# Performance work log

Measured on AMD Instinct MI355X. Metric: run time of the kernel, lower is better.

The kernel has to match this reference:

```python
import jax, jax.numpy as jnp
import numpy as np

B, T, D_IN, D_OUT = 4, 2048, 1024, 1024


def setup_inputs() -> dict:
    key = jax.random.key(0)
    k1, k2, k3, k4 = jax.random.split(key, 4)
    s_in = 1.0 / np.sqrt(D_IN)
    return {
        "input_vector": jax.random.normal(k1, (B, T, D_IN), dtype=jnp.float32),
        "w_q": jax.random.normal(k2, (D_IN, D_OUT), dtype=jnp.float32) * s_in,
        "w_k": jax.random.normal(k3, (D_IN, D_OUT), dtype=jnp.float32) * s_in,
        "w_v": jax.random.normal(k4, (D_IN, D_OUT), dtype=jnp.float32) * s_in,
    }


def reference(input_vector, w_q, w_k, w_v):
    # projections: [B, T, D_OUT]
    q = jnp.einsum("btd,de->bte", input_vector, w_q)
    k = jnp.einsum("btd,de->bte", input_vector, w_k)
    v = jnp.einsum("btd,de->bte", input_vector, w_v)

    T_ = q.shape[1]
    # raw scores [B, T, T]
    scores = jnp.einsum("bqd,bkd->bqk", q, k)
    # causal mask (strict upper triangle masked to -inf), applied BEFORE scaling
    # (as in the original; -inf is invariant under the scale anyway)
    causal = jnp.tril(jnp.ones((T_, T_), dtype=bool))  # True = keep
    scores = jnp.where(causal[None, :, :], scores, -jnp.inf)
    scores = scores / jnp.sqrt(jnp.asarray(k.shape[-1], scores.dtype))
    attn = jax.nn.softmax(scores, axis=-1)
    # dropout = 0.0 (eval): identity
    return jnp.einsum("bqk,bkd->bqd", attn, v)
```

## Files before the change

kernel.cpp:

```cpp
#include <hip/hip_runtime.h>
#include <cstdint>
#include <math.h>

typedef unsigned short u16;
typedef __attribute__((ext_vector_type(8))) short short8;
typedef __attribute__((ext_vector_type(16))) float f32x16;

__device__ __forceinline__ u16 f2bf(float f) {
  uint32_t u = __float_as_uint(f);
  u += 0x7FFFu + ((u >> 16) & 1u);
  return (u16)(u >> 16);
}
__device__ __forceinline__ float bf2f(u16 h) {
  return __uint_as_float(((uint32_t)h) << 16);
}

__device__ __forceinline__ void async_ld16(u16* lds, const u16* g) {
  __builtin_amdgcn_global_load_lds((const __attribute__((address_space(1))) uint32_t*)g,
                                   (__attribute__((address_space(3))) uint32_t*)lds,
                                   16, 0, 0);
}

template <bool OUT_BF16, int MODE, bool KLIM>
__global__ __launch_bounds__(256) void gemm_bt(
    const u16* __restrict__ A, int lda, long zsA,
    const u16* __restrict__ B, int ldb, long zsB,
    void* __restrict__ Cv, int ldc, long zsC,
    int K, float scale, int NB)
{
  const int b = blockIdx.x, zb = blockIdx.y;
  int nb, mb;
  if constexpr (MODE == 1) {
    const int u = b & 7, v = b >> 3;
    nb = v & (NB - 1);
    mb = u * ((int)(gridDim.x >> 3) / NB) + (v / NB);
  } else if constexpr (MODE == 2) {
    const int u = b & 7, idx = b >> 3;
    if (idx <= u) { mb = u;      nb = idx; }
    else          { mb = 15 - u; nb = idx - u - 1; }
  } else if constexpr (MODE == 3) {
    const int u = b & 7, idx = b >> 3;
    mb = (idx < 8) ? u : 15 - u;
    nb = idx & 7;
  } else {
    nb = b % NB;
    mb = b / NB;
  }

  A += (long)zb * zsA;
  B += (long)zb * zsB;
  const int m0 = mb * 128, n0 = nb * 128;

  __shared__ __align__(16) u16 lsA[128 * 32];
  __shared__ __align__(16) u16 lsB[128 * 32];

  const int tid = threadIdx.x;
  const int lane = tid & 63;
  const int wave = tid >> 6;
  const int wr = (wave >> 1) * 64;
  const int wc = (wave & 1) * 64;

  f32x16 acc[2][2];
#pragma unroll
  for (int i = 0; i < 2; ++i)
#pragma unroll
    for (int j = 0; j < 2; ++j)
#pragma unroll
      for (int r = 0; r < 16; ++r) acc[i][j][r] = 0.f;

  const int c0 = tid;
  const int c1 = tid + 256;
  const int r0 = c0 >> 2, q0 = (((c0 & 3) ^ (r0 & 3))) * 8;
  const int r1 = c1 >> 2, q1 = (((c1 & 3) ^ (r1 & 3))) * 8;

  const int klim = (mb + 1) * 128;
  const int kmax = KLIM ? (K < klim ? K : klim) : K;

  const u16* pA0 = A + (long)(m0 + r0) * lda + q0;
  const u16* pA1 = A + (long)(m0 + r1) * lda + q1;
  const u16* pB0 = B + (long)(n0 + r0) * ldb + q0;
  const u16* pB1 = B + (long)(n0 + r1) * ldb + q1;

  const int m32 = lane & 31;
  const int hh = lane >> 5;
  const int sw = lane & 3;
  int offA[2][2], offB[2][2];
#pragma unroll
  for (int i = 0; i < 2; ++i)
#pragma unroll
    for (int ks = 0; ks < 2; ++ks) {
      const int kq = ((ks << 1) | hh) ^ sw;
      offA[i][ks] = (wr + i * 32 + m32) * 32 + kq * 8;
      offB[i][ks] = (wc + i * 32 + m32) * 32 + kq * 8;
    }

  for (int k0 = 0; k0 < kmax; k0 += 32) {
    __syncthreads();
    async_ld16(&lsA[c0 * 8], pA0);
    async_ld16(&lsA[c1 * 8], pA1);
    async_ld16(&lsB[c0 * 8], pB0);
    async_ld16(&lsB[c1 * 8], pB1);
    pA0 += 32; pA1 += 32; pB0 += 32; pB1 += 32;
    __syncthreads();

#pragma unroll
    for (int ks = 0; ks < 2; ++ks) {
      const short8 a0 = *(const short8*)&lsA[offA[0][ks]];
      const short8 a1 = *(const short8*)&lsA[offA[1][ks]];
      const short8 b0 = *(const short8*)&lsB[offB[0][ks]];
      const short8 b1 = *(const short8*)&lsB[offB[1][ks]];
      acc[0][0] = __builtin_amdgcn_mfma_f32_32x32x16_bf16(a0, b0, acc[0][0], 0, 0, 0);
      acc[0][1] = __builtin_amdgcn_mfma_f32_32x32x16_bf16(a0, b1, acc[0][1], 0, 0, 0);
      acc[1][0] = __builtin_amdgcn_mfma_f32_32x32x16_bf16(a1, b0, acc[1][0], 0, 0, 0);
      acc[1][1] = __builtin_amdgcn_mfma_f32_32x32x16_bf16(a1, b1, acc[1][1], 0, 0, 0);
    }
  }

  const int ec = lane & 31;
  const int rb = (lane >> 5) * 4;

  if constexpr (OUT_BF16) {
    u16* C = (u16*)Cv + (long)zb * zsC;
#pragma unroll
    for (int i = 0; i < 2; ++i) {
      const int rbase = m0 + wr + i * 32 + rb;
#pragma unroll
      for (int j = 0; j < 2; ++j) {
        const int col = n0 + wc + j * 32 + ec;
#pragma unroll
        for (int r = 0; r < 16; ++r) {
          const int row = rbase + (r & 3) + 8 * (r >> 2);
          C[(long)row * ldc + col] = f2bf(acc[i][j][r] * scale);
        }
      }
    }
  } else {
    float* C = (float*)Cv + (long)zb * zsC;
#pragma unroll
    for (int i = 0; i < 2; ++i) {
      const int rbase = m0 + wr + i * 32 + rb;
#pragma unroll
      for (int j = 0; j < 2; ++j) {
        const int col = n0 + wc + j * 32 + ec;
#pragma unroll
        for (int r = 0; r < 16; ++r) {
          const int row = rbase + (r & 3) + 8 * (r >> 2);
          C[(long)row * ldc + col] = acc[i][j][r] * scale;
        }
      }
    }
  }
}

__global__ __launch_bounds__(256) void cast_x_kernel(const float* __restrict__ x,
                                                     u16* __restrict__ y) {
  const long i = ((long)blockIdx.x * 256 + threadIdx.x) * 4;
  const float4 v = *(const float4*)(x + i);
  ushort4 o;
  o.x = f2bf(v.x); o.y = f2bf(v.y); o.z = f2bf(v.z); o.w = f2bf(v.w);
  *(ushort4*)(y + i) = o;
}

__global__ __launch_bounds__(256) void cast_wt_kernel(const float* __restrict__ w0,
                                                      const float* __restrict__ w1,
                                                      const float* __restrict__ w2,
                                                      u16* __restrict__ Wt) {
  const float* W = (blockIdx.z == 0) ? w0 : (blockIdx.z == 1) ? w1 : w2;
  u16* o = Wt + (long)blockIdx.z * 1024 * 1024;
  __shared__ float t[32][33];
  const int n0 = blockIdx.x * 32, k0 = blockIdx.y * 32;
  const int tx = threadIdx.x, ty = threadIdx.y;
  for (int r = ty; r < 32; r += 8) t[r][tx] = W[(long)(k0 + r) * 1024 + n0 + tx];
  __syncthreads();
  for (int r = ty; r < 32; r += 8) o[(long)(n0 + r) * 1024 + k0 + tx] = f2bf(t[tx][r]);
}

__global__ __launch_bounds__(256) void transpose_v_kernel(const u16* __restrict__ V,
                                                          u16* __restrict__ Vt) {
  __shared__ u16 t[32][33];
  const int d0 = blockIdx.x * 32, t0 = blockIdx.y * 32, b = blockIdx.z;
  const u16* Vb = V + (long)b * 2048 * 1024;
  u16* Ob = Vt + (long)b * 1024 * 2048;
  const int tx = threadIdx.x, ty = threadIdx.y;
  for (int r = ty; r < 32; r += 8) t[r][tx] = Vb[(long)(t0 + r) * 1024 + d0 + tx];
  __syncthreads();
  for (int r = ty; r < 32; r += 8) Ob[(long)(d0 + r) * 2048 + t0 + tx] = t[tx][r];
}

__global__ __launch_bounds__(256) void softmax_rows(const u16* __restrict__ S,
                                                    u16* __restrict__ P, int T) {
  const int q = blockIdx.x, b = blockIdx.y;
  const u16* srow = S + ((long)b * T + q) * T;
  u16* prow = P + ((long)b * T + q) * T;
  const int L = q + 1;
  const int Lpad = ((q >> 7) + 1) << 7;
  const int tid = threadIdx.x;

  float sv[8];
  float m = -3.4e38f;
#pragma unroll
  for (int i = 0; i < 8; ++i) {
    const int j = tid + i * 256;
    sv[i] = (j < L) ? bf2f(srow[j]) : -3.4e38f;
    m = fmaxf(m, sv[i]);
  }
#pragma unroll
  for (int off = 32; off > 0; off >>= 1) m = fmaxf(m, __shfl_down(m, off, 64));

  __shared__ float red[4];
  __shared__ float bcast;
  if ((tid & 63) == 0) red[tid >> 6] = m;
  __syncthreads();
  if (tid == 0) bcast = fmaxf(fmaxf(red[0], red[1]), fmaxf(red[2], red[3]));
  __syncthreads();
  m = bcast;

  float s = 0.f;
#pragma unroll
  for (int i = 0; i < 8; ++i) {
    const int j = tid + i * 256;
    sv[i] = (j < L) ? __expf(sv[i] - m) : 0.f;
    s += sv[i];
  }
#pragma unroll
  for (int off = 32; off > 0; off >>= 1) s += __shfl_down(s, off, 64);
  __syncthreads();
  if ((tid & 63) == 0) red[tid >> 6] = s;
  __syncthreads();
  if (tid == 0) bcast = red[0] + red[1] + red[2] + red[3];
  __syncthreads();
  const float inv = 1.f / bcast;

#pragma unroll
  for (int i = 0; i < 8; ++i) {
    const int j = tid + i * 256;
    if (j < Lpad) prow[j] = f2bf(sv[i] * inv);
  }
}

extern "C" void kernel_launch(void* const* d_in, const int* in_sizes, int n_in,
                              void* d_out, int out_size, void* d_ws, size_t ws_size,
                              hipStream_t stream) {
  const float* X  = (const float*)d_in[0];
  const float* Wq = (const float*)d_in[1];
  const float* Wk = (const float*)d_in[2];
  const float* Wv = (const float*)d_in[3];
  float* out = (float*)d_out;

  const long BT = 8192;
  const long Tq = 2048, D = 1024;

  u16* Xbf = (u16*)d_ws;
  u16* Wt  = Xbf + BT * D;
  u16* QKV = Wt + 3 * D * D;
  u16* Vt  = QKV + 3 * BT * D;
  u16* Sb  = Vt + 4 * D * Tq;
  u16* P   = Sb + 4 * Tq * Tq;

  cast_x_kernel<<<8192, 256, 0, stream>>>(X, Xbf);
  cast_wt_kernel<<<dim3(32, 32, 3), dim3(32, 8), 0, stream>>>(Wq, Wk, Wv, Wt);

  gemm_bt<true, 1, false><<<dim3(512, 3), 256, 0, stream>>>(
      Xbf, 1024, 0L, Wt, 1024, D * D, QKV, 1024, BT * D, 1024, 1.0f, 8);

  gemm_bt<true, 2, false><<<dim3(136, 4), 256, 0, stream>>>(
      QKV, 1024, Tq * D, QKV + BT * D, 1024, Tq * D,
      Sb, 2048, Tq * Tq, 1024, 0.03125f, 16);

  softmax_rows<<<dim3(2048, 4), 256, 0, stream>>>(Sb, P, 2048);

  transpose_v_kernel<<<dim3(32, 64, 4), dim3(32, 8), 0, stream>>>(QKV + 2 * BT * D, Vt);

  gemm_bt<false, 3, true><<<dim3(128, 4), 256, 0, stream>>>(
      P, 2048, Tq * Tq, Vt, 2048, D * Tq,
      out, 1024, Tq * D, 2048, 1.0f, 8);
}
```

Measured before the change: 280.6 us.

## Double-buffer LDS tiles in bt GEMM and change the swizzle pattern

Allocates two LDS buffers per operand and prefetches the next K-slice with async global-to-LDS loads while MFMAs consume the current slice. This removes one barrier per iteration and overlaps global memory latency with compute. The LDS XOR swizzle now keys on row bits 1-2 instead of bits 0-1, to cut bank conflicts on the short8 reads. LDS use per block doubles, which may reduce occupancy, and correctness depends on the barrier waiting for the outstanding async loads.

```diff
diff --git a/kernel.cpp b/kernel.cpp
--- a/kernel.cpp
+++ b/kernel.cpp
@@ -51,8 +51,8 @@
   B += (long)zb * zsB;
   const int m0 = mb * 128, n0 = nb * 128;
 
-  __shared__ __align__(16) u16 lsA[128 * 32];
-  __shared__ __align__(16) u16 lsB[128 * 32];
+  __shared__ __align__(16) u16 lsA[2][128 * 32];
+  __shared__ __align__(16) u16 lsB[2][128 * 32];
 
   const int tid = threadIdx.x;
   const int lane = tid & 63;
@@ -70,8 +70,8 @@
 
   const int c0 = tid;
   const int c1 = tid + 256;
-  const int r0 = c0 >> 2, q0 = (((c0 & 3) ^ (r0 & 3))) * 8;
-  const int r1 = c1 >> 2, q1 = (((c1 & 3) ^ (r1 & 3))) * 8;
+  const int r0 = c0 >> 2, q0 = ((c0 & 3) ^ ((c0 >> 3) & 3)) * 8;
+  const int r1 = c1 >> 2, q1 = ((c1 & 3) ^ ((c1 >> 3) & 3)) * 8;
 
   const int klim = (mb + 1) * 128;
   const int kmax = KLIM ? (K < klim ? K : klim) : K;
@@ -83,37 +83,48 @@
 
   const int m32 = lane & 31;
   const int hh = lane >> 5;
-  const int sw = lane & 3;
+  const int rsw = (m32 >> 1) & 3;
   int offA[2][2], offB[2][2];
 #pragma unroll
   for (int i = 0; i < 2; ++i)
 #pragma unroll
     for (int ks = 0; ks < 2; ++ks) {
-      const int kq = ((ks << 1) | hh) ^ sw;
+      const int kq = ((ks << 1) | hh) ^ rsw;
       offA[i][ks] = (wr + i * 32 + m32) * 32 + kq * 8;
       offB[i][ks] = (wc + i * 32 + m32) * 32 + kq * 8;
     }
 
+  async_ld16(&lsA[0][c0 * 8], pA0);
+  async_ld16(&lsA[0][c1 * 8], pA1);
+  async_ld16(&lsB[0][c0 * 8], pB0);
+  async_ld16(&lsB[0][c1 * 8], pB1);
+  pA0 += 32; pA1 += 32; pB0 += 32; pB1 += 32;
+
+  int p = 0;
   for (int k0 = 0; k0 < kmax; k0 += 32) {
     __syncthreads();
-    async_ld16(&lsA[c0 * 8], pA0);
-    async_ld16(&lsA[c1 * 8], pA1);
-    async_ld16(&lsB[c0 * 8], pB0);
-    async_ld16(&lsB[c1 * 8], pB1);
-    pA0 += 32; pA1 += 32; pB0 += 32; pB1 += 32;
-    __syncthreads();
-
+    if (k0 + 32 < kmax) {
+      async_ld16(&lsA[p ^ 1][c0 * 8], pA0);
+      async_ld16(&lsA[p ^ 1][c1 * 8], pA1);
+      async_ld16(&lsB[p ^ 1][c0 * 8], pB0);
+      async_ld16(&lsB[p ^ 1][c1 * 8], pB1);
+      pA0 += 32; pA1 += 32; pB0 += 32; pB1 += 32;
+    }
+
+    const u16* la = lsA[p];
+    const u16* lb = lsB[p];
 #pragma unroll
     for (int ks = 0; ks < 2; ++ks) {
-      const short8 a0 = *(const short8*)&lsA[offA[0][ks]];
-      const short8 a1 = *(const short8*)&lsA[offA[1][ks]];
-      const short8 b0 = *(const short8*)&lsB[offB[0][ks]];
-      const short8 b1 = *(const short8*)&lsB[offB[1][ks]];
+      const short8 a0 = *(const short8*)&la[offA[0][ks]];
+      const short8 a1 = *(const short8*)&la[offA[1][ks]];
+      const short8 b0 = *(const short8*)&lb[offB[0][ks]];
+      const short8 b1 = *(const short8*)&lb[offB[1][ks]];
       acc[0][0] = __builtin_amdgcn_mfma_f32_32x32x16_bf16(a0, b0, acc[0][0], 0, 0, 0);
       acc[0][1] = __builtin_amdgcn_mfma_f32_32x32x16_bf16(a0, b1, acc[0][1], 0, 0, 0);
       acc[1][0] = __builtin_amdgcn_mfma_f32_32x32x16_bf16(a1, b0, acc[1][0], 0, 0, 0);
       acc[1][1] = __builtin_amdgcn_mfma_f32_32x32x16_bf16(a1, b1, acc[1][1], 0, 0, 0);
     }
+    p ^= 1;
   }
 
   const int ec = lane & 31;
```

After: 272.8 us. 2.8% less time.
